# Kernel optimization log

Hardware: AMD Instinct MI355X
Metric: run time of the kernel (lower is better)

The kernel has to match this reference:

```python
import jax, jax.numpy as jnp
import numpy as np

N = 100000   # nodes
E = 1600000  # edges
D = 128      # input feature dim
H1, H2 = 128, 128    # GCN hidden sizes
M1, M2 = 256, 128    # MLP hidden sizes
BN_EPS = 1e-5


def setup_inputs() -> dict:
    key = jax.random.key(0)
    ks = jax.random.split(key, 20)
    x = jax.random.normal(ks[0], (N, D), dtype=jnp.float32)
    edge_index = jax.random.randint(ks[1], (2, E), 0, N, dtype=jnp.int32)

    def lin(k, fi, fo):
        s = 1.0 / np.sqrt(fi)
        return jax.random.uniform(k, (fi, fo), jnp.float32, -s, s)

    inp = {"x": x, "edge_index": edge_index}
    inp["Wg1"] = lin(ks[2], D, H1);  inp["bg1"] = jnp.zeros((H1,), jnp.float32)
    inp["g1"]  = jnp.ones((H1,), jnp.float32); inp["be1"] = jnp.zeros((H1,), jnp.float32)
    inp["Wg2"] = lin(ks[3], H1, H2); inp["bg2"] = jnp.zeros((H2,), jnp.float32)
    inp["g2"]  = jnp.ones((H2,), jnp.float32); inp["be2"] = jnp.zeros((H2,), jnp.float32)
    inp["Wm1"] = lin(ks[4], H2, M1); inp["bm1"] = jnp.zeros((M1,), jnp.float32)
    inp["g3"]  = jnp.ones((M1,), jnp.float32); inp["be3"] = jnp.zeros((M1,), jnp.float32)
    inp["Wm2"] = lin(ks[5], M1, M2); inp["bm2"] = jnp.zeros((M2,), jnp.float32)
    inp["g4"]  = jnp.ones((M2,), jnp.float32); inp["be4"] = jnp.zeros((M2,), jnp.float32)
    inp["Wo"]  = lin(ks[6], M2, 1);  inp["bo"]  = jnp.zeros((1,), jnp.float32)
    return inp


def batch_norm(x, gamma, beta):
    # training-mode BatchNorm1d over the node/batch axis, biased variance
    mean = jnp.mean(x, axis=0)
    var = jnp.mean((x - mean) ** 2, axis=0)
    return (x - mean) * jax.lax.rsqrt(var + BN_EPS) * gamma + beta


def gcn_conv(x, src, dst, W, b):
    # PyG GCNConv: add self-loops, sym-normalize, aggregate (xW) over edges
    h = x @ W                                              # [N, F_out]
    deg = jnp.zeros((N,), x.dtype).at[dst].add(1.0) + 1.0  # in-degree + self-loop
    dinv = jax.lax.rsqrt(deg)
    coef = (dinv[src] * dinv[dst])[:, None]                # [E, 1]
    agg = jax.ops.segment_sum(h[src] * coef, dst, num_segments=N)
    agg = agg + h * (dinv * dinv)[:, None]                 # self-loop term
    return agg + b


def reference(x, edge_index, Wg1, bg1, g1, be1, Wg2, bg2, g2, be2,
              Wm1, bm1, g3, be3, Wm2, bm2, g4, be4, Wo, bo):
    src, dst = edge_index[0], edge_index[1]
    # GCN blocks: relu(dropout(bn(conv(x)))); dropout is identity in eval
    h = jax.nn.relu(batch_norm(gcn_conv(x, src, dst, Wg1, bg1), g1, be1))
    h = jax.nn.relu(batch_norm(gcn_conv(h, src, dst, Wg2, bg2), g2, be2))
    # MLP blocks
    h = jax.nn.relu(batch_norm(h @ Wm1 + bm1, g3, be3))
    h = jax.nn.relu(batch_norm(h @ Wm2 + bm2, g4, be4))
    return jax.nn.sigmoid(h @ Wo + bo)
```

## Files before the change

kernel.cpp:

```cpp
#include <hip/hip_runtime.h>
#include <hip/hip_bf16.h>
#include <math.h>


typedef __attribute__((ext_vector_type(8))) short bf16x8;
typedef __attribute__((ext_vector_type(4))) float f32x4;

__device__ inline void split2(float x, ushort& h, ushort& l) {
    unsigned u = __float_as_uint(x);
    h = (ushort)(u >> 16);
    float hb = __uint_as_float(u & 0xFFFF0000u);
    float lo = x - hb;
    unsigned b = __float_as_uint(lo);
    l = (ushort)((b + 0x7FFFu + ((b >> 16) & 1u)) >> 16);
}

__device__ inline void gload_lds16(const void* g, void* l) {
#if defined(__HIP_DEVICE_COMPILE__)
    __builtin_amdgcn_global_load_lds(
        (const __attribute__((address_space(1))) unsigned int*)g,
        (__attribute__((address_space(3))) unsigned int*)l, 16, 0, 0);
#endif
}

__global__ void degree_kernel(const int* __restrict__ dst, int* __restrict__ deg, int E) {
    int i = blockIdx.x * blockDim.x + threadIdx.x;
    if (i < E) atomicAdd(&deg[dst[i]], 1);
}

__global__ void dinv_kernel(const int* __restrict__ deg, float* __restrict__ dinv, int N) {
    int i = blockIdx.x * blockDim.x + threadIdx.x;
    if (i < N) dinv[i] = rsqrtf((float)(deg[i] + 1));
}

__global__ void blocksum_kernel(const int* __restrict__ deg, int* __restrict__ bsum, int N) {
    __shared__ int sh[256];
    int tid = threadIdx.x;
    int base = blockIdx.x * 1024 + tid * 4;
    int s = 0;
    #pragma unroll
    for (int j = 0; j < 4; ++j) { int idx = base + j; if (idx < N) s += deg[idx]; }
    sh[tid] = s; __syncthreads();
    for (int off = 128; off > 0; off >>= 1) {
        if (tid < off) sh[tid] += sh[tid + off];
        __syncthreads();
    }
    if (tid == 0) bsum[blockIdx.x] = sh[0];
}

__global__ void scan_bsum_kernel(int* bsum, int nb) {
    if (threadIdx.x == 0 && blockIdx.x == 0) {
        int run = 0;
        for (int i = 0; i < nb; ++i) { int v = bsum[i]; bsum[i] = run; run += v; }
    }
}

__global__ void scanwrite_kernel(const int* __restrict__ deg, const int* __restrict__ bsumex,
                                 int* __restrict__ row_ptr, int* __restrict__ cursor,
                                 int N, int Etot) {
    __shared__ int sh[256];
    int tid = threadIdx.x;
    int base = blockIdx.x * 1024 + tid * 4;
    int v[4]; int tsum = 0;
    #pragma unroll
    for (int j = 0; j < 4; ++j) { int idx = base + j; v[j] = (idx < N) ? deg[idx] : 0; tsum += v[j]; }
    sh[tid] = tsum; __syncthreads();
    for (int off = 1; off < 256; off <<= 1) {
        int x = (tid >= off) ? sh[tid - off] : 0;
        __syncthreads();
        sh[tid] += x;
        __syncthreads();
    }
    int run = sh[tid] - tsum + bsumex[blockIdx.x];
    #pragma unroll
    for (int j = 0; j < 4; ++j) {
        int idx = base + j;
        if (idx < N) { row_ptr[idx] = run; cursor[idx] = run; }
        run += v[j];
    }
    if (blockIdx.x == 0 && tid == 0) row_ptr[N] = Etot;
}

__global__ void scatter_kernel(const int* __restrict__ src, const int* __restrict__ dst,
                               const float* __restrict__ dinv,
                               int* __restrict__ cursor, uint2* __restrict__ esw, int E) {
    int i = blockIdx.x * blockDim.x + threadIdx.x;
    if (i < E) {
        int d = dst[i];
        int s = src[i];
        int pos = atomicAdd(&cursor[d], 1);
        esw[pos] = make_uint2((unsigned)s, __float_as_uint(dinv[s]));
    }
}

__global__ void wsplit_kernel(const float* __restrict__ W, ushort* __restrict__ Wh,
                              ushort* __restrict__ Wl, int FO) {
    int t = blockIdx.x * 256 + threadIdx.x;
    if (t >= 128 * FO) return;
    int j   = t & 7;
    int ci  = (t >> 3) & 127;
    int rest = t >> 10;
    int kg  = rest & 15;
    int cb  = rest >> 4;
    float w = W[(size_t)(kg * 8 + j) * FO + cb * 128 + ci];
    ushort h, l; split2(w, h, l);
    Wh[t] = h; Wl[t] = l;
}

template<bool ACT>
__global__ __launch_bounds__(256)
void actsplit_kernel(const float* __restrict__ X, char* __restrict__ A2,
                     const float* __restrict__ scale, const float* __restrict__ shift,
                     int nrows)
{
    int t = blockIdx.x * 256 + threadIdx.x;
    int r = t & 127;
    int kg = (t >> 7) & 3;
    int kstep = (t >> 9) & 3;
    int rowtile = t >> 11;
    int gr = rowtile * 128 + r;
    int k = kstep * 32 + kg * 8;
    float4 v0 = make_float4(0.f, 0.f, 0.f, 0.f), v1 = v0;
    if (gr < nrows) {
        v0 = *(const float4*)&X[(size_t)gr * 128 + k];
        v1 = *(const float4*)&X[(size_t)gr * 128 + k + 4];
        if (ACT) {
            float4 sc0 = *(const float4*)&scale[k],     sf0 = *(const float4*)&shift[k];
            float4 sc1 = *(const float4*)&scale[k + 4], sf1 = *(const float4*)&shift[k + 4];
            v0.x = fmaxf(fmaf(v0.x, sc0.x, sf0.x), 0.f);
            v0.y = fmaxf(fmaf(v0.y, sc0.y, sf0.y), 0.f);
            v0.z = fmaxf(fmaf(v0.z, sc0.z, sf0.z), 0.f);
            v0.w = fmaxf(fmaf(v0.w, sc0.w, sf0.w), 0.f);
            v1.x = fmaxf(fmaf(v1.x, sc1.x, sf1.x), 0.f);
            v1.y = fmaxf(fmaf(v1.y, sc1.y, sf1.y), 0.f);
            v1.z = fmaxf(fmaf(v1.z, sc1.z, sf1.z), 0.f);
            v1.w = fmaxf(fmaf(v1.w, sc1.w, sf1.w), 0.f);
        }
    }
    union { uint4 u; ushort s[8]; } ph, pl;
    split2(v0.x, ph.s[0], pl.s[0]); split2(v0.y, ph.s[1], pl.s[1]);
    split2(v0.z, ph.s[2], pl.s[2]); split2(v0.w, ph.s[3], pl.s[3]);
    split2(v1.x, ph.s[4], pl.s[4]); split2(v1.y, ph.s[5], pl.s[5]);
    split2(v1.z, ph.s[6], pl.s[6]); split2(v1.w, ph.s[7], pl.s[7]);
    char* base = A2 + ((size_t)(rowtile * 4 + kstep) * 16384) + kg * 2048 + r * 16;
    *(uint4*)base          = ph.u;
    *(uint4*)(base + 8192) = pl.u;
}

template<bool ACC>
__global__ __launch_bounds__(256)
void gemm_mfma_kernel(const char* __restrict__ A2, const ushort* __restrict__ W2h,
                      const ushort* __restrict__ W2l, float* __restrict__ C,
                      int nrows, int cbW)
{
    __shared__ char lds[16384];
    const int tid  = threadIdx.x;
    const int lane = tid & 63;
    const int wid  = tid >> 6;
    const int wm   = wid & 1, wn = wid >> 1;
    const int row0 = blockIdx.x * 128;
    const int l15  = lane & 15;
    const int l4   = lane >> 4;

    f32x4 zero = {0.f, 0.f, 0.f, 0.f};
    f32x4 acc[4][4];
    #pragma unroll
    for (int m = 0; m < 4; ++m)
        #pragma unroll
        for (int n = 0; n < 4; ++n) acc[m][n] = zero;

    const char* blob = A2 + ((size_t)blockIdx.x * 4) * 16384;

    for (int kstep = 0; kstep < 4; ++kstep) {
        const char* src = blob + (size_t)kstep * 16384;
        #pragma unroll
        for (int p = 0; p < 4; ++p) {
            gload_lds16(src + (((p * 4 + wid) * 64 + lane) * 16), &lds[(p * 4 + wid) * 1024]);
        }
        bf16x8 bh[4], bl[4];
        #pragma unroll
        for (int n = 0; n < 4; ++n) {
            int ci = wn * 64 + n * 16 + l15;
            size_t off = (((size_t)(cbW * 16 + kstep * 4 + l4)) * 128 + ci) * 8;
            bh[n] = *(const bf16x8*)&W2h[off];
            bl[n] = *(const bf16x8*)&W2l[off];
        }
        __syncthreads();
        bf16x8 ah[4], al[4];
        #pragma unroll
        for (int m = 0; m < 4; ++m) {
            int o = l4 * 2048 + (wm * 64 + m * 16 + l15) * 16;
            ah[m] = *(const bf16x8*)&lds[o];
            al[m] = *(const bf16x8*)&lds[o + 8192];
        }
        #pragma unroll
        for (int m = 0; m < 4; ++m)
            #pragma unroll
            for (int n = 0; n < 4; ++n) {
                acc[m][n] = __builtin_amdgcn_mfma_f32_16x16x32_bf16(ah[m], bh[n], acc[m][n], 0, 0, 0);
                acc[m][n] = __builtin_amdgcn_mfma_f32_16x16x32_bf16(ah[m], bl[n], acc[m][n], 0, 0, 0);
                acc[m][n] = __builtin_amdgcn_mfma_f32_16x16x32_bf16(al[m], bh[n], acc[m][n], 0, 0, 0);
            }
        __syncthreads();
    }

    #pragma unroll
    for (int m = 0; m < 4; ++m) {
        int rbase = row0 + wm * 64 + m * 16 + l4 * 4;
        #pragma unroll
        for (int r = 0; r < 4; ++r) {
            int gr = rbase + r;
            if (gr < nrows) {
                #pragma unroll
                for (int n = 0; n < 4; ++n) {
                    int gc = wn * 64 + n * 16 + l15;
                    size_t idx = (size_t)gr * 128 + gc;
                    if (ACC) C[idx] += acc[m][n][r];
                    else     C[idx]  = acc[m][n][r];
                }
            }
        }
    }
}

__global__ void agg_kernel(const float* __restrict__ T, float* __restrict__ Aout,
                           const float* __restrict__ dinv,
                           const int* __restrict__ row_ptr, const uint2* __restrict__ esw,
                           int nrows)
{
    int gw = (blockIdx.x * blockDim.x + threadIdx.x) >> 6;
    int lane = threadIdx.x & 63;
    int nw = (gridDim.x * blockDim.x) >> 6;
    int c = lane * 2;
    for (int i = gw; i < nrows; i += nw) {
        float di = dinv[i];
        int e0 = __builtin_amdgcn_readfirstlane(row_ptr[i]);
        int e1 = __builtin_amdgcn_readfirstlane(row_ptr[i + 1]);
        float ax0 = 0.f, ay0 = 0.f, ax1 = 0.f, ay1 = 0.f;
        int e = e0;
        int eq = e0 + ((e1 - e0) & ~3);
        for (; e < eq; e += 4) {
            uint2 p0 = esw[e],     p1 = esw[e + 1];
            uint2 p2 = esw[e + 2], p3 = esw[e + 3];
            float2 v0 = *(const float2*)&T[((size_t)p0.x << 7) + c];
            float2 v1 = *(const float2*)&T[((size_t)p1.x << 7) + c];
            float2 v2 = *(const float2*)&T[((size_t)p2.x << 7) + c];
            float2 v3 = *(const float2*)&T[((size_t)p3.x << 7) + c];
            float w0 = __uint_as_float(p0.y), w1 = __uint_as_float(p1.y);
            float w2 = __uint_as_float(p2.y), w3 = __uint_as_float(p3.y);
            ax0 = fmaf(w0, v0.x, ax0); ay0 = fmaf(w0, v0.y, ay0);
            ax1 = fmaf(w1, v1.x, ax1); ay1 = fmaf(w1, v1.y, ay1);
            ax0 = fmaf(w2, v2.x, ax0); ay0 = fmaf(w2, v2.y, ay0);
            ax1 = fmaf(w3, v3.x, ax1); ay1 = fmaf(w3, v3.y, ay1);
        }
        for (; e < e1; ++e) {
            uint2 p = esw[e];
            float w = __uint_as_float(p.y);
            float2 v = *(const float2*)&T[((size_t)p.x << 7) + c];
            ax0 = fmaf(w, v.x, ax0); ay0 = fmaf(w, v.y, ay0);
        }
        float ax = ax0 + ax1, ay = ay0 + ay1;
        float2 self = *(const float2*)&T[((size_t)i << 7) + c];
        float2 o;
        o.x = fmaf(di, ax, di * di * self.x);
        o.y = fmaf(di, ay, di * di * self.y);
        *(float2*)&Aout[((size_t)i << 7) + c] = o;
    }
}

__global__ void colstats_kernel(const float* __restrict__ X, int nrows, int rpb,
                                float* __restrict__ colsum, float* __restrict__ colsq)
{
    __shared__ float ss[256], sq[256];
    int tid = threadIdx.x;
    int c = tid & 127;
    int roff = tid >> 7;
    int r0 = blockIdx.x * rpb;
    int r1 = min(nrows, r0 + rpb);
    float s = 0.f, q = 0.f;
    for (int r = r0 + roff; r < r1; r += 2) {
        float v = X[(size_t)r * 128 + c];
        s += v; q += v * v;
    }
    ss[tid] = s; sq[tid] = q;
    __syncthreads();
    if (tid < 128) {
        float S = ss[tid] + ss[tid + 128];
        float Q = sq[tid] + sq[tid + 128];
        atomicAdd(&colsum[tid], S);
        atomicAdd(&colsq[tid], Q);
    }
}

__global__ void bnparam_kernel(const float* __restrict__ colsum, const float* __restrict__ colsq,
                               const float* __restrict__ g, const float* __restrict__ be,
                               float* __restrict__ scale, float* __restrict__ shift,
                               float invN)
{
    int c = threadIdx.x;
    if (c < 128) {
        float mean = colsum[c] * invN;
        float var = colsq[c] * invN - mean * mean;
        float rs = rsqrtf(var + 1e-5f);
        float sc = g[c] * rs;
        scale[c] = sc;
        shift[c] = be[c] - mean * sc;
    }
}

__global__ void final_kernel(const float* __restrict__ A, const float* __restrict__ Wo,
                             const float* __restrict__ bo,
                             const float* __restrict__ scale, const float* __restrict__ shift,
                             float* __restrict__ out, int nrows)
{
    int gw = (blockIdx.x * blockDim.x + threadIdx.x) >> 6;
    int lane = threadIdx.x & 63;
    int nw = (gridDim.x * blockDim.x) >> 6;
    int c = lane * 2;
    float2 w = *(const float2*)&Wo[c];
    float2 sc = *(const float2*)&scale[c];
    float2 sf = *(const float2*)&shift[c];
    float bias = bo[0];
    for (int i = gw; i < nrows; i += nw) {
        float2 v = *(const float2*)&A[(size_t)i * 128 + c];
        float x = fmaxf(fmaf(v.x, sc.x, sf.x), 0.f) * w.x
                + fmaxf(fmaf(v.y, sc.y, sf.y), 0.f) * w.y;
        #pragma unroll
        for (int off = 32; off > 0; off >>= 1) x += __shfl_down(x, off);
        if (lane == 0) out[i] = 1.f / (1.f + expf(-(x + bias)));
    }
}

extern "C" void kernel_launch(void* const* d_in, const int* in_sizes, int n_in,
                              void* d_out, int out_size, void* d_ws, size_t ws_size,
                              hipStream_t stream)
{
    const float* x   = (const float*)d_in[0];
    const int* ei    = (const int*)d_in[1];
    const float* Wg1 = (const float*)d_in[2];
    const float* g1  = (const float*)d_in[4];
    const float* be1 = (const float*)d_in[5];
    const float* Wg2 = (const float*)d_in[6];
    const float* g2  = (const float*)d_in[8];
    const float* be2 = (const float*)d_in[9];
    const float* Wm1 = (const float*)d_in[10];
    const float* g3  = (const float*)d_in[12];
    const float* be3 = (const float*)d_in[13];
    const float* Wm2 = (const float*)d_in[14];
    const float* g4  = (const float*)d_in[16];
    const float* be4 = (const float*)d_in[17];
    const float* Wo  = (const float*)d_in[18];
    const float* bo  = (const float*)d_in[19];

    const int N = in_sizes[0] / 128;
    const int E = in_sizes[1] / 2;
    const int* srcv = ei;
    const int* dstv = ei + E;
    const int rowtiles = (N + 127) / 128;
    const size_t blobsz = (size_t)rowtiles * 4 * 16384;

    char* p = (char*)d_ws;
    auto alloc = [&](size_t bytes) { void* r = (void*)p; p += (bytes + 255) & ~(size_t)255; return r; };
    float* buf1    = (float*)alloc((size_t)N * 128 * 4);
    char*  buf2    = (char*)alloc(blobsz);
    char*  buf3    = (char*)alloc(blobsz);
    int*   deg     = (int*)alloc((size_t)N * 4);
    float* dinv    = (float*)alloc((size_t)N * 4);
    int*   row_ptr = (int*)alloc((size_t)(N + 1) * 4);
    int*   cursor  = (int*)alloc((size_t)N * 4);
    uint2* esw     = (uint2*)alloc((size_t)(E + 8) * 8);
    int*   bsum    = (int*)alloc(4096);
    float* colsum  = (float*)alloc(512 * 4);
    float* colsq   = colsum + 128;
    float* scale   = (float*)alloc(256 * 4);
    float* shift   = (float*)alloc(256 * 4);
    ushort* W2h    = (ushort*)alloc(32768 * 2);
    ushort* W2l    = (ushort*)alloc(32768 * 2);

    float* Abuf = (float*)buf2;
    float* C4   = (float*)buf3;
    const int rpb = (N + 255) / 256;
    const float invN = 1.f / (float)N;
    const int as_blocks = rowtiles * 8;

    (void)hipMemsetAsync(deg, 0, (size_t)N * 4, stream);
    degree_kernel<<<(E + 255) / 256, 256, 0, stream>>>(dstv, deg, E);
    dinv_kernel<<<(N + 255) / 256, 256, 0, stream>>>(deg, dinv, N);
    int nb = (N + 1023) / 1024;
    blocksum_kernel<<<nb, 256, 0, stream>>>(deg, bsum, N);
    scan_bsum_kernel<<<1, 64, 0, stream>>>(bsum, nb);
    scanwrite_kernel<<<nb, 256, 0, stream>>>(deg, bsum, row_ptr, cursor, N, E);
    scatter_kernel<<<(E + 255) / 256, 256, 0, stream>>>(srcv, dstv, dinv, cursor, esw, E);

    dim3 gg(rowtiles, 1);

    wsplit_kernel<<<64, 256, 0, stream>>>(Wg1, W2h, W2l, 128);
    actsplit_kernel<false><<<as_blocks, 256, 0, stream>>>(x, buf3, nullptr, nullptr, N);
    gemm_mfma_kernel<false><<<gg, 256, 0, stream>>>(buf3, W2h, W2l, buf1, N, 0);
    agg_kernel<<<2048, 256, 0, stream>>>(buf1, Abuf, dinv, row_ptr, esw, N);
    (void)hipMemsetAsync(colsum, 0, 256 * 4, stream);
    colstats_kernel<<<256, 256, 0, stream>>>(Abuf, N, rpb, colsum, colsq);
    bnparam_kernel<<<1, 128, 0, stream>>>(colsum, colsq, g1, be1, scale, shift, invN);

    wsplit_kernel<<<64, 256, 0, stream>>>(Wg2, W2h, W2l, 128);
    actsplit_kernel<true><<<as_blocks, 256, 0, stream>>>(Abuf, buf3, scale, shift, N);
    gemm_mfma_kernel<false><<<gg, 256, 0, stream>>>(buf3, W2h, W2l, buf1, N, 0);
    agg_kernel<<<2048, 256, 0, stream>>>(buf1, Abuf, dinv, row_ptr, esw, N);
    (void)hipMemsetAsync(colsum, 0, 256 * 4, stream);
    colstats_kernel<<<256, 256, 0, stream>>>(Abuf, N, rpb, colsum, colsq);
    bnparam_kernel<<<1, 128, 0, stream>>>(colsum, colsq, g2, be2, scale, shift, invN);

    actsplit_kernel<true><<<as_blocks, 256, 0, stream>>>(Abuf, buf3, scale, shift, N);
    wsplit_kernel<<<128, 256, 0, stream>>>(Wm1, W2h, W2l, 256);

    gemm_mfma_kernel<false><<<gg, 256, 0, stream>>>(buf3, W2h, W2l, buf1, N, 0);
    (void)hipMemsetAsync(colsum, 0, 256 * 4, stream);
    colstats_kernel<<<256, 256, 0, stream>>>(buf1, N, rpb, colsum, colsq);
    bnparam_kernel<<<1, 128, 0, stream>>>(colsum, colsq, g3, be3, scale, shift, invN);
    actsplit_kernel<true><<<as_blocks, 256, 0, stream>>>(buf1, buf2, scale, shift, N);

    gemm_mfma_kernel<false><<<gg, 256, 0, stream>>>(buf3, W2h, W2l, buf1, N, 1);
    (void)hipMemsetAsync(colsum, 0, 256 * 4, stream);
    colstats_kernel<<<256, 256, 0, stream>>>(buf1, N, rpb, colsum, colsq);
    bnparam_kernel<<<1, 128, 0, stream>>>(colsum, colsq, g3 + 128, be3 + 128, scale, shift, invN);

    wsplit_kernel<<<64, 256, 0, stream>>>(Wm2, W2h, W2l, 128);
    gemm_mfma_kernel<false><<<gg, 256, 0, stream>>>(buf2, W2h, W2l, C4, N, 0);

    actsplit_kernel<true><<<as_blocks, 256, 0, stream>>>(buf1, buf2, scale, shift, N);
    wsplit_kernel<<<64, 256, 0, stream>>>(Wm2 + 128 * 128, W2h, W2l, 128);
    gemm_mfma_kernel<true><<<gg, 256, 0, stream>>>(buf2, W2h, W2l, C4, N, 0);

    (void)hipMemsetAsync(colsum, 0, 256 * 4, stream);
    colstats_kernel<<<256, 256, 0, stream>>>(C4, N, rpb, colsum, colsq);
    bnparam_kernel<<<1, 128, 0, stream>>>(colsum, colsq, g4, be4, scale, shift, invN);
    final_kernel<<<1024, 256, 0, stream>>>(C4, Wo, bo, scale, shift, (float*)d_out, N);
}
```

Baseline: 1.069 ms.

## Fuse BatchNorm statistics into GEMM and aggregation epilogues, drop stats kernels

Column sum and sum-of-squares are now accumulated inside the aggregation and GEMM epilogues with atomics, and the BN scale/shift are recomputed on the fly in the consumers. This removes the separate colstats and bnparam launches, their memsets, and a full re-read of each activation. The dinv computation is folded into the scan kernel, all stat buffers are zeroed with one memset, the GEMM loads its whole A tile into 64KB LDS at once instead of per k-step, and the aggregation loop is unrolled to 8 edges. The larger LDS footprint may reduce occupancy, and per-block float atomics make the statistics order-dependent.

```diff
diff --git a/kernel.cpp b/kernel.cpp
--- a/kernel.cpp
+++ b/kernel.cpp
@@ -28,11 +28,6 @@
     if (i < E) atomicAdd(&deg[dst[i]], 1);
 }
 
-__global__ void dinv_kernel(const int* __restrict__ deg, float* __restrict__ dinv, int N) {
-    int i = blockIdx.x * blockDim.x + threadIdx.x;
-    if (i < N) dinv[i] = rsqrtf((float)(deg[i] + 1));
-}
-
 __global__ void blocksum_kernel(const int* __restrict__ deg, int* __restrict__ bsum, int N) {
     __shared__ int sh[256];
     int tid = threadIdx.x;
@@ -57,7 +52,7 @@
 
 __global__ void scanwrite_kernel(const int* __restrict__ deg, const int* __restrict__ bsumex,
                                  int* __restrict__ row_ptr, int* __restrict__ cursor,
-                                 int N, int Etot) {
+                                 float* __restrict__ dinv, int N, int Etot) {
     __shared__ int sh[256];
     int tid = threadIdx.x;
     int base = blockIdx.x * 1024 + tid * 4;
@@ -75,7 +70,10 @@
     #pragma unroll
     for (int j = 0; j < 4; ++j) {
         int idx = base + j;
-        if (idx < N) { row_ptr[idx] = run; cursor[idx] = run; }
+        if (idx < N) {
+            row_ptr[idx] = run; cursor[idx] = run;
+            dinv[idx] = rsqrtf((float)(v[j] + 1));
+        }
         run += v[j];
     }
     if (blockIdx.x == 0 && tid == 0) row_ptr[N] = Etot;
@@ -110,8 +108,9 @@
 template<bool ACT>
 __global__ __launch_bounds__(256)
 void actsplit_kernel(const float* __restrict__ X, char* __restrict__ A2,
-                     const float* __restrict__ scale, const float* __restrict__ shift,
-                     int nrows)
+                     const float* __restrict__ csum, const float* __restrict__ csq,
+                     const float* __restrict__ g, const float* __restrict__ be,
+                     float invN, int nrows)
 {
     int t = blockIdx.x * 256 + threadIdx.x;
     int r = t & 127;
@@ -125,16 +124,20 @@
         v0 = *(const float4*)&X[(size_t)gr * 128 + k];
         v1 = *(const float4*)&X[(size_t)gr * 128 + k + 4];
         if (ACT) {
-            float4 sc0 = *(const float4*)&scale[k],     sf0 = *(const float4*)&shift[k];
-            float4 sc1 = *(const float4*)&scale[k + 4], sf1 = *(const float4*)&shift[k + 4];
-            v0.x = fmaxf(fmaf(v0.x, sc0.x, sf0.x), 0.f);
-            v0.y = fmaxf(fmaf(v0.y, sc0.y, sf0.y), 0.f);
-            v0.z = fmaxf(fmaf(v0.z, sc0.z, sf0.z), 0.f);
-            v0.w = fmaxf(fmaf(v0.w, sc0.w, sf0.w), 0.f);
-            v1.x = fmaxf(fmaf(v1.x, sc1.x, sf1.x), 0.f);
-            v1.y = fmaxf(fmaf(v1.y, sc1.y, sf1.y), 0.f);
-            v1.z = fmaxf(fmaf(v1.z, sc1.z, sf1.z), 0.f);
-            v1.w = fmaxf(fmaf(v1.w, sc1.w, sf1.w), 0.f);
+            float4 s0 = *(const float4*)&csum[k], s1 = *(const float4*)&csum[k + 4];
+            float4 q0 = *(const float4*)&csq[k],  q1 = *(const float4*)&csq[k + 4];
+            float4 g0 = *(const float4*)&g[k],    g1v = *(const float4*)&g[k + 4];
+            float4 b0 = *(const float4*)&be[k],   b1 = *(const float4*)&be[k + 4];
+            #define BN1(vv, ss, qq, gg, bb) { \
+                float mean = (ss) * invN; \
+                float var = (qq) * invN - mean * mean; \
+                float sc = (gg) * rsqrtf(var + 1e-5f); \
+                (vv) = fmaxf(fmaf((vv), sc, (bb) - mean * sc), 0.f); }
+            BN1(v0.x, s0.x, q0.x, g0.x, b0.x) BN1(v0.y, s0.y, q0.y, g0.y, b0.y)
+            BN1(v0.z, s0.z, q0.z, g0.z, b0.z) BN1(v0.w, s0.w, q0.w, g0.w, b0.w)
+            BN1(v1.x, s1.x, q1.x, g1v.x, b1.x) BN1(v1.y, s1.y, q1.y, g1v.y, b1.y)
+            BN1(v1.z, s1.z, q1.z, g1v.z, b1.z) BN1(v1.w, s1.w, q1.w, g1v.w, b1.w)
+            #undef BN1
         }
     }
     union { uint4 u; ushort s[8]; } ph, pl;
@@ -147,13 +150,13 @@
     *(uint4*)(base + 8192) = pl.u;
 }
 
-template<bool ACC>
+template<bool ACC, bool STATS>
 __global__ __launch_bounds__(256)
 void gemm_mfma_kernel(const char* __restrict__ A2, const ushort* __restrict__ W2h,
                       const ushort* __restrict__ W2l, float* __restrict__ C,
-                      int nrows, int cbW)
+                      int nrows, int cbW, float* __restrict__ csum, float* __restrict__ csq)
 {
-    __shared__ char lds[16384];
+    __shared__ char lds[65536];
     const int tid  = threadIdx.x;
     const int lane = tid & 63;
     const int wid  = tid >> 6;
@@ -162,6 +165,13 @@
     const int l15  = lane & 15;
     const int l4   = lane >> 4;
 
+    const char* blob = A2 + (size_t)blockIdx.x * 65536;
+    #pragma unroll
+    for (int j = 0; j < 16; ++j) {
+        int plane = wid * 16 + j;
+        gload_lds16(blob + plane * 1024 + lane * 16, &lds[plane * 1024]);
+    }
+
     f32x4 zero = {0.f, 0.f, 0.f, 0.f};
     f32x4 acc[4][4];
     #pragma unroll
@@ -169,14 +179,11 @@
         #pragma unroll
         for (int n = 0; n < 4; ++n) acc[m][n] = zero;
 
-    const char* blob = A2 + ((size_t)blockIdx.x * 4) * 16384;
-
+    __syncthreads();
+
+    #pragma unroll
     for (int kstep = 0; kstep < 4; ++kstep) {
-        const char* src = blob + (size_t)kstep * 16384;
-        #pragma unroll
-        for (int p = 0; p < 4; ++p) {
-            gload_lds16(src + (((p * 4 + wid) * 64 + lane) * 16), &lds[(p * 4 + wid) * 1024]);
-        }
+        const int kbase = kstep * 16384;
         bf16x8 bh[4], bl[4];
         #pragma unroll
         for (int n = 0; n < 4; ++n) {
@@ -185,11 +192,10 @@
             bh[n] = *(const bf16x8*)&W2h[off];
             bl[n] = *(const bf16x8*)&W2l[off];
         }
-        __syncthreads();
         bf16x8 ah[4], al[4];
         #pragma unroll
         for (int m = 0; m < 4; ++m) {
-            int o = l4 * 2048 + (wm * 64 + m * 16 + l15) * 16;
+            int o = kbase + l4 * 2048 + (wm * 64 + m * 16 + l15) * 16;
             ah[m] = *(const bf16x8*)&lds[o];
             al[m] = *(const bf16x8*)&lds[o + 8192];
         }
@@ -201,9 +207,9 @@
                 acc[m][n] = __builtin_amdgcn_mfma_f32_16x16x32_bf16(ah[m], bl[n], acc[m][n], 0, 0, 0);
                 acc[m][n] = __builtin_amdgcn_mfma_f32_16x16x32_bf16(al[m], bh[n], acc[m][n], 0, 0, 0);
             }
-        __syncthreads();
-    }
-
+    }
+
+    float s[4] = {0.f, 0.f, 0.f, 0.f}, q[4] = {0.f, 0.f, 0.f, 0.f};
     #pragma unroll
     for (int m = 0; m < 4; ++m) {
         int rbase = row0 + wm * 64 + m * 16 + l4 * 4;
@@ -215,9 +221,26 @@
                 for (int n = 0; n < 4; ++n) {
                     int gc = wn * 64 + n * 16 + l15;
                     size_t idx = (size_t)gr * 128 + gc;
-                    if (ACC) C[idx] += acc[m][n][r];
-                    else     C[idx]  = acc[m][n][r];
+                    float v = acc[m][n][r];
+                    if (ACC) v += C[idx];
+                    C[idx] = v;
+                    if (STATS) { s[n] += v; q[n] += v * v; }
                 }
+            }
+        }
+    }
+    if (STATS) {
+        #pragma unroll
+        for (int n = 0; n < 4; ++n) {
+            s[n] += __shfl_xor(s[n], 16); s[n] += __shfl_xor(s[n], 32);
+            q[n] += __shfl_xor(q[n], 16); q[n] += __shfl_xor(q[n], 32);
+        }
+        if (l4 == 0) {
+            #pragma unroll
+            for (int n = 0; n < 4; ++n) {
+                int col = wn * 64 + n * 16 + l15;
+                atomicAdd(&csum[col], s[n]);
+                atomicAdd(&csq[col], q[n]);
             }
         }
     }
@@ -226,32 +249,35 @@
 __global__ void agg_kernel(const float* __restrict__ T, float* __restrict__ Aout,
                            const float* __restrict__ dinv,
                            const int* __restrict__ row_ptr, const uint2* __restrict__ esw,
-                           int nrows)
+                           int nrows, float* __restrict__ csum, float* __restrict__ csq)
 {
+    __shared__ float sred[1024];
+    int lane = threadIdx.x & 63;
+    int wid = threadIdx.x >> 6;
     int gw = (blockIdx.x * blockDim.x + threadIdx.x) >> 6;
-    int lane = threadIdx.x & 63;
     int nw = (gridDim.x * blockDim.x) >> 6;
     int c = lane * 2;
+    float sx = 0.f, sy = 0.f, qx = 0.f, qy = 0.f;
     for (int i = gw; i < nrows; i += nw) {
         float di = dinv[i];
         int e0 = __builtin_amdgcn_readfirstlane(row_ptr[i]);
         int e1 = __builtin_amdgcn_readfirstlane(row_ptr[i + 1]);
         float ax0 = 0.f, ay0 = 0.f, ax1 = 0.f, ay1 = 0.f;
         int e = e0;
-        int eq = e0 + ((e1 - e0) & ~3);
-        for (; e < eq; e += 4) {
-            uint2 p0 = esw[e],     p1 = esw[e + 1];
-            uint2 p2 = esw[e + 2], p3 = esw[e + 3];
-            float2 v0 = *(const float2*)&T[((size_t)p0.x << 7) + c];
-            float2 v1 = *(const float2*)&T[((size_t)p1.x << 7) + c];
-            float2 v2 = *(const float2*)&T[((size_t)p2.x << 7) + c];
-            float2 v3 = *(const float2*)&T[((size_t)p3.x << 7) + c];
-            float w0 = __uint_as_float(p0.y), w1 = __uint_as_float(p1.y);
-            float w2 = __uint_as_float(p2.y), w3 = __uint_as_float(p3.y);
-            ax0 = fmaf(w0, v0.x, ax0); ay0 = fmaf(w0, v0.y, ay0);
-            ax1 = fmaf(w1, v1.x, ax1); ay1 = fmaf(w1, v1.y, ay1);
-            ax0 = fmaf(w2, v2.x, ax0); ay0 = fmaf(w2, v2.y, ay0);
-            ax1 = fmaf(w3, v3.x, ax1); ay1 = fmaf(w3, v3.y, ay1);
+        int n8 = e0 + ((e1 - e0) & ~7);
+        for (; e < n8; e += 8) {
+            uint2 p[8];
+            #pragma unroll
+            for (int j = 0; j < 8; ++j) p[j] = esw[e + j];
+            float2 v[8];
+            #pragma unroll
+            for (int j = 0; j < 8; ++j) v[j] = *(const float2*)&T[((size_t)p[j].x << 7) + c];
+            #pragma unroll
+            for (int j = 0; j < 8; ++j) {
+                float w = __uint_as_float(p[j].y);
+                if (j & 1) { ax1 = fmaf(w, v[j].x, ax1); ay1 = fmaf(w, v[j].y, ay1); }
+                else       { ax0 = fmaf(w, v[j].x, ax0); ay0 = fmaf(w, v[j].y, ay0); }
+            }
         }
         for (; e < e1; ++e) {
             uint2 p = esw[e];
@@ -265,66 +291,49 @@
         o.x = fmaf(di, ax, di * di * self.x);
         o.y = fmaf(di, ay, di * di * self.y);
         *(float2*)&Aout[((size_t)i << 7) + c] = o;
-    }
-}
-
-__global__ void colstats_kernel(const float* __restrict__ X, int nrows, int rpb,
-                                float* __restrict__ colsum, float* __restrict__ colsq)
-{
-    __shared__ float ss[256], sq[256];
-    int tid = threadIdx.x;
-    int c = tid & 127;
-    int roff = tid >> 7;
-    int r0 = blockIdx.x * rpb;
-    int r1 = min(nrows, r0 + rpb);
-    float s = 0.f, q = 0.f;
-    for (int r = r0 + roff; r < r1; r += 2) {
-        float v = X[(size_t)r * 128 + c];
-        s += v; q += v * v;
-    }
-    ss[tid] = s; sq[tid] = q;
+        sx += o.x; sy += o.y;
+        qx += o.x * o.x; qy += o.y * o.y;
+    }
+    int si = (wid * 64 + lane) * 4;
+    sred[si] = sx; sred[si + 1] = sy; sred[si + 2] = qx; sred[si + 3] = qy;
     __syncthreads();
-    if (tid < 128) {
-        float S = ss[tid] + ss[tid + 128];
-        float Q = sq[tid] + sq[tid + 128];
-        atomicAdd(&colsum[tid], S);
-        atomicAdd(&colsq[tid], Q);
-    }
-}
-
-__global__ void bnparam_kernel(const float* __restrict__ colsum, const float* __restrict__ colsq,
-                               const float* __restrict__ g, const float* __restrict__ be,
-                               float* __restrict__ scale, float* __restrict__ shift,
-                               float invN)
-{
-    int c = threadIdx.x;
-    if (c < 128) {
-        float mean = colsum[c] * invN;
-        float var = colsq[c] * invN - mean * mean;
-        float rs = rsqrtf(var + 1e-5f);
-        float sc = g[c] * rs;
-        scale[c] = sc;
-        shift[c] = be[c] - mean * sc;
+    if (wid == 0) {
+        float a0 = 0.f, a1 = 0.f, a2 = 0.f, a3 = 0.f;
+        #pragma unroll
+        for (int w = 0; w < 4; ++w) {
+            int b = (w * 64 + lane) * 4;
+            a0 += sred[b]; a1 += sred[b + 1]; a2 += sred[b + 2]; a3 += sred[b + 3];
+        }
+        atomicAdd(&csum[c], a0);     atomicAdd(&csum[c + 1], a1);
+        atomicAdd(&csq[c], a2);      atomicAdd(&csq[c + 1], a3);
     }
 }
 
 __global__ void final_kernel(const float* __restrict__ A, const float* __restrict__ Wo,
                              const float* __restrict__ bo,
-                             const float* __restrict__ scale, const float* __restrict__ shift,
-                             float* __restrict__ out, int nrows)
+                             const float* __restrict__ csum, const float* __restrict__ csq,
+                             const float* __restrict__ g, const float* __restrict__ be,
+                             float invN, float* __restrict__ out, int nrows)
 {
     int gw = (blockIdx.x * blockDim.x + threadIdx.x) >> 6;
     int lane = threadIdx.x & 63;
     int nw = (gridDim.x * blockDim.x) >> 6;
     int c = lane * 2;
     float2 w = *(const float2*)&Wo[c];
-    float2 sc = *(const float2*)&scale[c];
-    float2 sf = *(const float2*)&shift[c];
+    float2 sm = *(const float2*)&csum[c];
+    float2 sq = *(const float2*)&csq[c];
+    float2 gg = *(const float2*)&g[c];
+    float2 bb = *(const float2*)&be[c];
+    float mean0 = sm.x * invN, mean1 = sm.y * invN;
+    float sc0 = gg.x * rsqrtf(sq.x * invN - mean0 * mean0 + 1e-5f);
+    float sc1 = gg.y * rsqrtf(sq.y * invN - mean1 * mean1 + 1e-5f);
+    float sf0 = bb.x - mean0 * sc0;
+    float sf1 = bb.y - mean1 * sc1;
     float bias = bo[0];
     for (int i = gw; i < nrows; i += nw) {
         float2 v = *(const float2*)&A[(size_t)i * 128 + c];
-        float x = fmaxf(fmaf(v.x, sc.x, sf.x), 0.f) * w.x
-                + fmaxf(fmaf(v.y, sc.y, sf.y), 0.f) * w.y;
+        float x = fmaxf(fmaf(v.x, sc0, sf0), 0.f) * w.x
+                + fmaxf(fmaf(v.y, sc1, sf1), 0.f) * w.y;
         #pragma unroll
         for (int off = 32; off > 0; off >>= 1) x += __shfl_down(x, off);
         if (lane == 0) out[i] = 1.f / (1.f + expf(-(x + bias)));
@@ -364,75 +373,60 @@
     float* buf1    = (float*)alloc((size_t)N * 128 * 4);
     char*  buf2    = (char*)alloc(blobsz);
     char*  buf3    = (char*)alloc(blobsz);
-    int*   deg     = (int*)alloc((size_t)N * 4);
+    const size_t degB = ((size_t)N * 4 + 15) & ~(size_t)15;
+    char*  zreg    = (char*)alloc(degB + 5 * 1024);
+    int*   deg     = (int*)zreg;
+    float* SB      = (float*)(zreg + degB);
     float* dinv    = (float*)alloc((size_t)N * 4);
     int*   row_ptr = (int*)alloc((size_t)(N + 1) * 4);
     int*   cursor  = (int*)alloc((size_t)N * 4);
     uint2* esw     = (uint2*)alloc((size_t)(E + 8) * 8);
     int*   bsum    = (int*)alloc(4096);
-    float* colsum  = (float*)alloc(512 * 4);
-    float* colsq   = colsum + 128;
-    float* scale   = (float*)alloc(256 * 4);
-    float* shift   = (float*)alloc(256 * 4);
     ushort* W2h    = (ushort*)alloc(32768 * 2);
     ushort* W2l    = (ushort*)alloc(32768 * 2);
 
+    float* S1 = SB,        *S1q = SB + 128;
+    float* S2 = SB + 256,  *S2q = SB + 384;
+    float* S3a = SB + 512, *S3aq = SB + 640;
+    float* S3b = SB + 768, *S3bq = SB + 896;
+    float* S4 = SB + 1024, *S4q = SB + 1152;
+
     float* Abuf = (float*)buf2;
     float* C4   = (float*)buf3;
-    const int rpb = (N + 255) / 256;
     const float invN = 1.f / (float)N;
     const int as_blocks = rowtiles * 8;
 
-    (void)hipMemsetAsync(deg, 0, (size_t)N * 4, stream);
+    (void)hipMemsetAsync(zreg, 0, degB + 5 * 1024, stream);
     degree_kernel<<<(E + 255) / 256, 256, 0, stream>>>(dstv, deg, E);
-    dinv_kernel<<<(N + 255) / 256, 256, 0, stream>>>(deg, dinv, N);
     int nb = (N + 1023) / 1024;
     blocksum_kernel<<<nb, 256, 0, stream>>>(deg, bsum, N);
     scan_bsum_kernel<<<1, 64, 0, stream>>>(bsum, nb);
-    scanwrite_kernel<<<nb, 256, 0, stream>>>(deg, bsum, row_ptr, cursor, N, E);
+    scanwrite_kernel<<<nb, 256, 0, stream>>>(deg, bsum, row_ptr, cursor, dinv, N, E);
     scatter_kernel<<<(E + 255) / 256, 256, 0, stream>>>(srcv, dstv, dinv, cursor, esw, E);
 
     dim3 gg(rowtiles, 1);
 
     wsplit_kernel<<<64, 256, 0, stream>>>(Wg1, W2h, W2l, 128);
-    actsplit_kernel<false><<<as_blocks, 256, 0, stream>>>(x, buf3, nullptr, nullptr, N);
-    gemm_mfma_kernel<false><<<gg, 256, 0, stream>>>(buf3, W2h, W2l, buf1, N, 0);
-    agg_kernel<<<2048, 256, 0, stream>>>(buf1, Abuf, dinv, row_ptr, esw, N);
-    (void)hipMemsetAsync(colsum, 0, 256 * 4, stream);
-    colstats_kernel<<<256, 256, 0, stream>>>(Abuf, N, rpb, colsum, colsq);
-    bnparam_kernel<<<1, 128, 0, stream>>>(colsum, colsq, g1, be1, scale, shift, invN);
+    actsplit_kernel<false><<<as_blocks, 256, 0, stream>>>(x, buf3, nullptr, nullptr, nullptr, nullptr, invN, N);
+    gemm_mfma_kernel<false, false><<<gg, 256, 0, stream>>>(buf3, W2h, W2l, buf1, N, 0, nullptr, nullptr);
+    agg_kernel<<<2048, 256, 0, stream>>>(buf1, Abuf, dinv, row_ptr, esw, N, S1, S1q);
 
     wsplit_kernel<<<64, 256, 0, stream>>>(Wg2, W2h, W2l, 128);
-    actsplit_kernel<true><<<as_blocks, 256, 0, stream>>>(Abuf, buf3, scale, shift, N);
-    gemm_mfma_kernel<false><<<gg, 256, 0, stream>>>(buf3, W2h, W2l, buf1, N, 0);
-    agg_kernel<<<2048, 256, 0, stream>>>(buf1, Abuf, dinv, row_ptr, esw, N);
-    (void)hipMemsetAsync(colsum, 0, 256 * 4, stream);
-    colstats_kernel<<<256, 256, 0, stream>>>(Abuf, N, rpb, colsum, colsq);
-    bnparam_kernel<<<1, 128, 0, stream>>>(colsum, colsq, g2, be2, scale, shift, invN);
-
-    actsplit_kernel<true><<<as_blocks, 256, 0, stream>>>(Abuf, buf3, scale, shift, N);
+    actsplit_kernel<true><<<as_blocks, 256, 0, stream>>>(Abuf, buf3, S1, S1q, g1, be1, invN, N);
+    gemm_mfma_kernel<false, false><<<gg, 256, 0, stream>>>(buf3, W2h, W2l, buf1, N, 0, nullptr, nullptr);
+    agg_kernel<<<2048, 256, 0, stream>>>(buf1, Abuf, dinv, row_ptr, esw, N, S2, S2q);
+
+    actsplit_kernel<true><<<as_blocks, 256, 0, stream>>>(Abuf, buf3, S2, S2q, g2, be2, invN, N);
     wsplit_kernel<<<128, 256, 0, stream>>>(Wm1, W2h, W2l, 256);
-
-    gemm_mfma_kernel<false><<<gg, 256, 0, stream>>>(buf3, W2h, W2l, buf1, N, 0);
-    (void)hipMemsetAsync(colsum, 0, 256 * 4, stream);
-    colstats_kernel<<<256, 256, 0, stream>>>(buf1, N, rpb, colsum, colsq);
-    bnparam_kernel<<<1, 128, 0, stream>>>(colsum, colsq, g3, be3, scale, shift, invN);
-    actsplit_kernel<true><<<as_blocks, 256, 0, stream>>>(buf1, buf2, scale, shift, N);
-
-    gemm_mfma_kernel<false><<<gg, 256, 0, stream>>>(buf3, W2h, W2l, buf1, N, 1);
-    (void)hipMemsetAsync(colsum, 0, 256 * 4, stream);
-    colstats_kernel<<<256, 256, 0, stream>>>(buf1, N, rpb, colsum, colsq);
-    bnparam_kernel<<<1, 128, 0, stream>>>(colsum, colsq, g3 + 128, be3 + 128, scale, shift, invN);
+    gemm_mfma_kernel<false, true><<<gg, 256, 0, stream>>>(buf3, W2h, W2l, buf1, N, 0, S3a, S3aq);
+    actsplit_kernel<true><<<as_blocks, 256, 0, stream>>>(buf1, buf2, S3a, S3aq, g3, be3, invN, N);
+    gemm_mfma_kernel<false, true><<<gg, 256, 0, stream>>>(buf3, W2h, W2l, buf1, N, 1, S3b, S3bq);
 
     wsplit_kernel<<<64, 256, 0, stream>>>(Wm2, W2h, W2l, 128);
-    gemm_mfma_kernel<false><<<gg, 256, 0, stream>>>(buf2, W2h, W2l, C4, N, 0);
-
-    actsplit_kernel<true><<<as_blocks, 256, 0, stream>>>(buf1, buf2, scale, shift, N);
+    gemm_mfma_kernel<false, false><<<gg, 256, 0, stream>>>(buf2, W2h, W2l, C4, N, 0, nullptr, nullptr);
+    actsplit_kernel<true><<<as_blocks, 256, 0, stream>>>(buf1, buf2, S3b, S3bq, g3 + 128, be3 + 128, invN, N);
     wsplit_kernel<<<64, 256, 0, stream>>>(Wm2 + 128 * 128, W2h, W2l, 128);
-    gemm_mfma_kernel<true><<<gg, 256, 0, stream>>>(buf2, W2h, W2l, C4, N, 0);
-
-    (void)hipMemsetAsync(colsum, 0, 256 * 4, stream);
-    colstats_kernel<<<256, 256, 0, stream>>>(C4, N, rpb, colsum, colsq);
-    bnparam_kernel<<<1, 128, 0, stream>>>(colsum, colsq, g4, be4, scale, shift, invN);
-    final_kernel<<<1024, 256, 0, stream>>>(C4, Wo, bo, scale, shift, (float*)d_out, N);
-}
+    gemm_mfma_kernel<true, true><<<gg, 256, 0, stream>>>(buf2, W2h, W2l, C4, N, 0, S4, S4q);
+
+    final_kernel<<<1024, 256, 0, stream>>>(C4, Wo, bo, S4, S4q, g4, be4, invN, (float*)d_out, N);
+}
```

Measured after the change: 1.060 ms. About the same (-0.9%).
